# Optimization experiments

Measured on AMD Instinct MI355X. Metric: run time of the kernel, lower is better.

The kernel has to match this reference:

```python
import jax, jax.numpy as jnp
import numpy as np

SNR_DB = 20.0   # fixed draw from snr_range=(20, 20)
B_COEF = 0.02   # pink-noise IIR coefficient


def setup_inputs() -> dict:
    key = jax.random.key(0)
    k1, k2 = jax.random.split(key)
    L = 16_777_216  # 2**24 audio samples
    audio = jax.random.normal(k1, (L,), dtype=jnp.float32)
    white = jax.random.normal(k2, (L,), dtype=jnp.float32)  # driving white noise for pink branch
    return {"audio": audio, "white": white}


def _pink_noise(white):
    # p[0] = 0; p[i] = B*w[i] + (1-B)*p[i-1]  -> linear recurrence x_i = a_i*x_{i-1} + u_i
    b = jnp.asarray(B_COEF, white.dtype)
    a = jnp.full(white.shape, 1.0 - B_COEF, white.dtype).at[0].set(0.0)
    u = (b * white).at[0].set(0.0)

    def combine(lhs, rhs):
        a1, u1 = lhs
        a2, u2 = rhs
        return a1 * a2, a2 * u1 + u2

    _, pink = jax.lax.associative_scan(combine, (a, u))
    return pink


def reference(audio, white):
    signal_power = jnp.mean(audio ** 2)
    noise_power = signal_power / (10.0 ** (SNR_DB / 10.0))
    noise = _pink_noise(white) * jnp.sqrt(noise_power)
    return audio + noise
```

## Files before the change

kernel.cpp:

```cpp
#include <hip/hip_runtime.h>
#include <math.h>

#define L_TOTAL (1 << 24)

constexpr float A_COEF = 0.98f;
constexpr float B_COEF = 0.02f;

constexpr int T    = 256;
constexpr int TS   = 4096;
constexpr int WARM = 512;
constexpr int NPART = 1024;

__device__ __forceinline__ void block_sync_lds() {
    asm volatile("s_waitcnt lgkmcnt(0)\n\ts_barrier" ::: "memory");
}

__global__ __launch_bounds__(256) void sumsq_kernel(const float4* __restrict__ a4,
                                                    float* __restrict__ partials,
                                                    int n4) {
    int idx    = blockIdx.x * blockDim.x + threadIdx.x;
    int stride = gridDim.x * blockDim.x;
    float s = 0.f;
    for (int i = idx; i < n4; i += stride) {
        float4 v = a4[i];
        s += v.x * v.x + v.y * v.y + v.z * v.z + v.w * v.w;
    }
    #pragma unroll
    for (int o = 32; o > 0; o >>= 1) s += __shfl_down(s, o, 64);
    __shared__ float wsum[4];
    int lane = threadIdx.x & 63;
    int wv   = threadIdx.x >> 6;
    if (lane == 0) wsum[wv] = s;
    __syncthreads();
    if (threadIdx.x == 0)
        partials[blockIdx.x] = wsum[0] + wsum[1] + wsum[2] + wsum[3];
}

__global__ __launch_bounds__(256) void pink_add_kernel(const float* __restrict__ audio,
                                                       const float* __restrict__ white,
                                                       const float* __restrict__ partials,
                                                       float* __restrict__ out) {
    __shared__ float gtot[4][4];
    __shared__ float wsum[4];
    __shared__ float psum[4];

    const int tid  = threadIdx.x;
    const int lane = tid & 63;
    const int wv   = tid >> 6;
    const int base = blockIdx.x * TS;

    const float4* wp4 = reinterpret_cast<const float4*>(white + base);
    float4 u[4];
    #pragma unroll
    for (int q = 0; q < 4; ++q) u[q] = wp4[q * T + tid];

    float2 wu = make_float2(0.f, 0.f);
    if (blockIdx.x > 0) {
        const float2* up = reinterpret_cast<const float2*>(white + base - WARM);
        wu = up[tid];
    }
    const float4 pp = reinterpret_cast<const float4*>(partials)[tid];

    const float4* ap4 = reinterpret_cast<const float4*>(audio + base);
    float4 av[4];
    #pragma unroll
    for (int q = 0; q < 4; ++q) av[q] = ap4[q * T + tid];

    const float a2c  = A_COEF * A_COEF;
    const float b4c  = a2c * a2c;
    const float b8c  = b4c * b4c, b16c = b8c * b8c, b32c = b16c * b16c;
    const float b64c = b32c * b32c, b128c = b64c * b64c;
    const float b256c  = b128c * b128c;
    const float b1024c = b256c * b256c * b256c * b256c;
    const float bpow[6] = {b4c, b8c, b16c, b32c, b64c, b128c};
    const float cg[4] = {1.f, b1024c, b1024c * b1024c, b1024c * b1024c * b1024c};

    const float b4lane = exp2f((float)lane * log2f(b4c));
    float b256w = 1.f;
    #pragma unroll
    for (int i = 0; i < 3; ++i) if (wv > i) b256w *= b256c;
    const float b4t = b4lane * b256w;

    #pragma unroll
    for (int q = 0; q < 4; ++q) {
        u[q].x *= B_COEF; u[q].y *= B_COEF; u[q].z *= B_COEF; u[q].w *= B_COEF;
    }
    if (base == 0 && tid == 0) u[0].x = 0.f;

    float W[4];
    #pragma unroll
    for (int q = 0; q < 4; ++q) {
        float p = u[q].x;
        p = fmaf(A_COEF, p, u[q].y);
        p = fmaf(A_COEF, p, u[q].z);
        p = fmaf(A_COEF, p, u[q].w);
        W[q] = p;
    }

    #pragma unroll
    for (int i = 0; i < 6; ++i) {
        const int o = 1 << i;
        #pragma unroll
        for (int q = 0; q < 4; ++q) {
            float up = __shfl_up(W[q], o, 64);
            if (lane >= o) W[q] = fmaf(bpow[i], up, W[q]);
        }
    }

    float part = fmaf(A_COEF, B_COEF * wu.x, B_COEF * wu.y);
    part *= exp2f((float)(255 - tid) * log2f(a2c));
    #pragma unroll
    for (int o = 32; o > 0; o >>= 1) part += __shfl_down(part, o, 64);

    float ss = pp.x + pp.y + pp.z + pp.w;
    #pragma unroll
    for (int o = 32; o > 0; o >>= 1) ss += __shfl_down(ss, o, 64);

    if (lane == 63) {
        #pragma unroll
        for (int q = 0; q < 4; ++q) gtot[q][wv] = W[q];
    }
    if (lane == 0) { wsum[wv] = part; psum[wv] = ss; }
    block_sync_lds();

    float P[4], Gt[4];
    #pragma unroll
    for (int q = 0; q < 4; ++q) {
        const float G0 = gtot[q][0], G1 = gtot[q][1];
        const float G2 = gtot[q][2], G3 = gtot[q][3];
        const float P1 = G0;
        const float P2 = fmaf(P1, b256c, G1);
        const float P3 = fmaf(P2, b256c, G2);
        P[q]  = (wv == 0) ? 0.f : (wv == 1) ? P1 : (wv == 2) ? P2 : P3;
        Gt[q] = fmaf(P3, b256c, G3);
    }
    const float Cw    = wsum[0] + wsum[1] + wsum[2] + wsum[3];
    const float sumsq = psum[0] + psum[1] + psum[2] + psum[3];
    const float scale = sqrtf(sumsq * (1.0f / ((float)L_TOTAL * 100.0f)));

    float H[4];
    H[0] = 0.f;
    H[1] = Gt[0];
    H[2] = fmaf(H[1], b1024c, Gt[1]);
    H[3] = fmaf(H[2], b1024c, Gt[2]);

    float4* op4 = reinterpret_cast<float4*>(out + base);
    #pragma unroll
    for (int q = 0; q < 4; ++q) {
        const float Wp = __shfl_up(W[q], 1, 64);
        const float E  = ((lane == 0) ? 0.f : Wp) + P[q] * b4lane;
        const float C  = E + fmaf(Cw, cg[q], H[q] / 1.0f) * b4t
                           - H[q] * b4t + (H[q] + Cw * cg[q]) * b4t;
        const float Cx = E + (H[q] + Cw * cg[q]) * b4t;

        float p = Cx;
        float4 r;
        p = fmaf(A_COEF, p, u[q].x); r.x = fmaf(p, scale, av[q].x);
        p = fmaf(A_COEF, p, u[q].y); r.y = fmaf(p, scale, av[q].y);
        p = fmaf(A_COEF, p, u[q].z); r.z = fmaf(p, scale, av[q].z);
        p = fmaf(A_COEF, p, u[q].w); r.w = fmaf(p, scale, av[q].w);
        (void)C;
        op4[q * T + tid] = r;
    }
}

extern "C" void kernel_launch(void* const* d_in, const int* in_sizes, int n_in,
                              void* d_out, int out_size, void* d_ws, size_t ws_size,
                              hipStream_t stream) {
    const float* audio = (const float*)d_in[0];
    const float* white = (const float*)d_in[1];
    float* out         = (float*)d_out;
    float* partials    = (float*)d_ws;

    const int n4 = L_TOTAL / 4;
    sumsq_kernel<<<NPART, 256, 0, stream>>>((const float4*)audio, partials, n4);

    const int blocks = L_TOTAL / TS;
    pink_add_kernel<<<blocks, 256, 0, stream>>>(audio, white, partials, out);
}
```

Before: 169.0 us.

## Fuse sum-of-squares and pink-noise passes into one cooperative grid-synced kernel

Replaces the two-kernel sequence with a single cooperative kernel of 2048 blocks. Each block first reduces its own slice of audio into a partial, then does a grid-wide sync, rebuilds the global scale, and processes two 4096-sample tiles of the pink-noise scan plus add. The goal is to drop one kernel launch and to reuse audio the block just read, which may still sit in cache. In exchange it relies on 2048 blocks being co-resident (occupancy hint of 8 per CU), pays for a grid barrier, and falls back to the old two-kernel path if the cooperative launch fails.

```diff
diff --git a/kernel.cpp b/kernel.cpp
--- a/kernel.cpp
+++ b/kernel.cpp
@@ -1,18 +1,185 @@
 #include <hip/hip_runtime.h>
+#include <hip/hip_cooperative_groups.h>
 #include <math.h>
+
+namespace cg = cooperative_groups;
 
 #define L_TOTAL (1 << 24)
 
 constexpr float A_COEF = 0.98f;
 constexpr float B_COEF = 0.02f;
 
-constexpr int T    = 256;
-constexpr int TS   = 4096;
-constexpr int WARM = 512;
+constexpr int T     = 256;
+constexpr int TS    = 4096;
+constexpr int SUB   = 2;
+constexpr int BS    = TS * SUB;
+constexpr int NBLK  = L_TOTAL / BS;
+constexpr int WARM  = 512;
 constexpr int NPART = 1024;
 
 __device__ __forceinline__ void block_sync_lds() {
     asm volatile("s_waitcnt lgkmcnt(0)\n\ts_barrier" ::: "memory");
+}
+
+__global__ __launch_bounds__(256, 8) void fused_kernel(const float* __restrict__ audio,
+                                                       const float* __restrict__ white,
+                                                       float* __restrict__ out,
+                                                       float* __restrict__ partials) {
+    __shared__ float red[4];
+    __shared__ float s_scale;
+    __shared__ float gtot[4][4];
+    __shared__ float wsum[4];
+
+    const int tid  = threadIdx.x;
+    const int lane = tid & 63;
+    const int wv   = tid >> 6;
+    const int b    = blockIdx.x;
+
+    {
+        const float4* a4 = reinterpret_cast<const float4*>(audio) + (size_t)b * (BS / 4);
+        float s = 0.f;
+        #pragma unroll
+        for (int i = 0; i < BS / (4 * T); ++i) {
+            float4 v = a4[i * T + tid];
+            s += v.x * v.x + v.y * v.y + v.z * v.z + v.w * v.w;
+        }
+        #pragma unroll
+        for (int o = 32; o > 0; o >>= 1) s += __shfl_down(s, o, 64);
+        if (lane == 0) red[wv] = s;
+        __syncthreads();
+        if (tid == 0) partials[b] = red[0] + red[1] + red[2] + red[3];
+    }
+    __threadfence();
+    cg::this_grid().sync();
+
+    {
+        const float4* p4 = reinterpret_cast<const float4*>(partials);
+        float4 x = p4[tid];
+        float4 y = p4[T + tid];
+        float ss = x.x + x.y + x.z + x.w + y.x + y.y + y.z + y.w;
+        #pragma unroll
+        for (int o = 32; o > 0; o >>= 1) ss += __shfl_down(ss, o, 64);
+        if (lane == 0) red[wv] = ss;
+        __syncthreads();
+        if (tid == 0)
+            s_scale = sqrtf((red[0] + red[1] + red[2] + red[3]) *
+                            (1.0f / ((float)L_TOTAL * 100.0f)));
+        __syncthreads();
+    }
+    const float scale = s_scale;
+
+    constexpr float a2c    = A_COEF * A_COEF;
+    constexpr float b4c    = a2c * a2c;
+    constexpr float b8c    = b4c * b4c;
+    constexpr float b16c   = b8c * b8c;
+    constexpr float b32c   = b16c * b16c;
+    constexpr float b64c   = b32c * b32c;
+    constexpr float b128c  = b64c * b64c;
+    constexpr float b256c  = b128c * b128c;
+    constexpr float b1024c = b256c * b256c * b256c * b256c;
+    const float bpow[6] = {b4c, b8c, b16c, b32c, b64c, b128c};
+    const float cgf[4]  = {1.f, b1024c, b1024c * b1024c, b1024c * b1024c * b1024c};
+
+    const float b4lane = exp2f((float)lane * log2f(b4c));
+    float b256w = 1.f;
+    #pragma unroll
+    for (int i = 0; i < 3; ++i) if (wv > i) b256w *= b256c;
+    const float b4t  = b4lane * b256w;
+    const float wexp = exp2f((float)(255 - tid) * log2f(a2c));
+
+    for (int sidx = 0; sidx < SUB; ++sidx) {
+        const int base = b * BS + sidx * TS;
+
+        const float4* wp4 = reinterpret_cast<const float4*>(white + base);
+        float4 u[4];
+        #pragma unroll
+        for (int q = 0; q < 4; ++q) u[q] = wp4[q * T + tid];
+
+        float2 wu = make_float2(0.f, 0.f);
+        if (base > 0) {
+            const float2* up = reinterpret_cast<const float2*>(white + base - WARM);
+            wu = up[tid];
+        }
+
+        #pragma unroll
+        for (int q = 0; q < 4; ++q) {
+            u[q].x *= B_COEF; u[q].y *= B_COEF; u[q].z *= B_COEF; u[q].w *= B_COEF;
+        }
+        if (base == 0 && tid == 0) u[0].x = 0.f;
+
+        float W[4];
+        #pragma unroll
+        for (int q = 0; q < 4; ++q) {
+            float p = u[q].x;
+            p = fmaf(A_COEF, p, u[q].y);
+            p = fmaf(A_COEF, p, u[q].z);
+            p = fmaf(A_COEF, p, u[q].w);
+            W[q] = p;
+        }
+
+        #pragma unroll
+        for (int i = 0; i < 6; ++i) {
+            const int o = 1 << i;
+            #pragma unroll
+            for (int q = 0; q < 4; ++q) {
+                float up = __shfl_up(W[q], o, 64);
+                if (lane >= o) W[q] = fmaf(bpow[i], up, W[q]);
+            }
+        }
+
+        float part = fmaf(A_COEF, B_COEF * wu.x, B_COEF * wu.y) * wexp;
+        #pragma unroll
+        for (int o = 32; o > 0; o >>= 1) part += __shfl_down(part, o, 64);
+
+        if (lane == 63) {
+            #pragma unroll
+            for (int q = 0; q < 4; ++q) gtot[q][wv] = W[q];
+        }
+        if (lane == 0) wsum[wv] = part;
+
+        const float4* ap4 = reinterpret_cast<const float4*>(audio + base);
+        float4 av[4];
+        #pragma unroll
+        for (int q = 0; q < 4; ++q) av[q] = ap4[q * T + tid];
+
+        block_sync_lds();
+
+        float P[4], Gt[4];
+        #pragma unroll
+        for (int q = 0; q < 4; ++q) {
+            const float G0 = gtot[q][0], G1 = gtot[q][1];
+            const float G2 = gtot[q][2], G3 = gtot[q][3];
+            const float P1 = G0;
+            const float P2 = fmaf(P1, b256c, G1);
+            const float P3 = fmaf(P2, b256c, G2);
+            P[q]  = (wv == 0) ? 0.f : (wv == 1) ? P1 : (wv == 2) ? P2 : P3;
+            Gt[q] = fmaf(P3, b256c, G3);
+        }
+        const float Cw = wsum[0] + wsum[1] + wsum[2] + wsum[3];
+
+        float H[4];
+        H[0] = 0.f;
+        H[1] = Gt[0];
+        H[2] = fmaf(H[1], b1024c, Gt[1]);
+        H[3] = fmaf(H[2], b1024c, Gt[2]);
+
+        float4* op4 = reinterpret_cast<float4*>(out + base);
+        #pragma unroll
+        for (int q = 0; q < 4; ++q) {
+            const float Wp = __shfl_up(W[q], 1, 64);
+            const float E  = ((lane == 0) ? 0.f : Wp) + P[q] * b4lane;
+            const float Cx = E + (H[q] + Cw * cgf[q]) * b4t;
+
+            float p = Cx;
+            float4 r;
+            p = fmaf(A_COEF, p, u[q].x); r.x = fmaf(p, scale, av[q].x);
+            p = fmaf(A_COEF, p, u[q].y); r.y = fmaf(p, scale, av[q].y);
+            p = fmaf(A_COEF, p, u[q].z); r.z = fmaf(p, scale, av[q].z);
+            p = fmaf(A_COEF, p, u[q].w); r.w = fmaf(p, scale, av[q].w);
+            op4[q * T + tid] = r;
+        }
+        block_sync_lds();
+    }
 }
 
 __global__ __launch_bounds__(256) void sumsq_kernel(const float4* __restrict__ a4,
@@ -66,14 +233,17 @@
     #pragma unroll
     for (int q = 0; q < 4; ++q) av[q] = ap4[q * T + tid];
 
-    const float a2c  = A_COEF * A_COEF;
-    const float b4c  = a2c * a2c;
-    const float b8c  = b4c * b4c, b16c = b8c * b8c, b32c = b16c * b16c;
-    const float b64c = b32c * b32c, b128c = b64c * b64c;
-    const float b256c  = b128c * b128c;
-    const float b1024c = b256c * b256c * b256c * b256c;
+    constexpr float a2c    = A_COEF * A_COEF;
+    constexpr float b4c    = a2c * a2c;
+    constexpr float b8c    = b4c * b4c;
+    constexpr float b16c   = b8c * b8c;
+    constexpr float b32c   = b16c * b16c;
+    constexpr float b64c   = b32c * b32c;
+    constexpr float b128c  = b64c * b64c;
+    constexpr float b256c  = b128c * b128c;
+    constexpr float b1024c = b256c * b256c * b256c * b256c;
     const float bpow[6] = {b4c, b8c, b16c, b32c, b64c, b128c};
-    const float cg[4] = {1.f, b1024c, b1024c * b1024c, b1024c * b1024c * b1024c};
+    const float cgf[4]  = {1.f, b1024c, b1024c * b1024c, b1024c * b1024c * b1024c};
 
     const float b4lane = exp2f((float)lane * log2f(b4c));
     float b256w = 1.f;
@@ -149,9 +319,7 @@
     for (int q = 0; q < 4; ++q) {
         const float Wp = __shfl_up(W[q], 1, 64);
         const float E  = ((lane == 0) ? 0.f : Wp) + P[q] * b4lane;
-        const float C  = E + fmaf(Cw, cg[q], H[q] / 1.0f) * b4t
-                           - H[q] * b4t + (H[q] + Cw * cg[q]) * b4t;
-        const float Cx = E + (H[q] + Cw * cg[q]) * b4t;
+        const float Cx = E + (H[q] + Cw * cgf[q]) * b4t;
 
         float p = Cx;
         float4 r;
@@ -159,7 +327,6 @@
         p = fmaf(A_COEF, p, u[q].y); r.y = fmaf(p, scale, av[q].y);
         p = fmaf(A_COEF, p, u[q].z); r.z = fmaf(p, scale, av[q].z);
         p = fmaf(A_COEF, p, u[q].w); r.w = fmaf(p, scale, av[q].w);
-        (void)C;
         op4[q * T + tid] = r;
     }
 }
@@ -172,9 +339,13 @@
     float* out         = (float*)d_out;
     float* partials    = (float*)d_ws;
 
-    const int n4 = L_TOTAL / 4;
-    sumsq_kernel<<<NPART, 256, 0, stream>>>((const float4*)audio, partials, n4);
-
-    const int blocks = L_TOTAL / TS;
-    pink_add_kernel<<<blocks, 256, 0, stream>>>(audio, white, partials, out);
-}
+    void* args[] = {(void*)&audio, (void*)&white, (void*)&out, (void*)&partials};
+    hipError_t err = hipLaunchCooperativeKernel((const void*)fused_kernel,
+                                                dim3(NBLK), dim3(T), args, 0, stream);
+    if (err != hipSuccess) {
+        (void)hipGetLastError();
+        const int n4 = L_TOTAL / 4;
+        sumsq_kernel<<<NPART, 256, 0, stream>>>((const float4*)audio, partials, n4);
+        pink_add_kernel<<<L_TOTAL / TS, 256, 0, stream>>>(audio, white, partials, out);
+    }
+}
```

After: 567.0 us. 235% more time.
